# Optimization experiments

Hardware: AMD Instinct MI355X
Metric: run time of the kernel (lower is better)

The kernel has to match this reference:

```python
import jax, jax.numpy as jnp
import numpy as np

B, IMG, CIN, COUT = 8, 256, 64, 64
TILE_NUM, KSIZE = 4, 5
TILE = IMG // TILE_NUM                 # 64
FFT = KSIZE + TILE - 1                 # 68
PAD = (FFT - TILE) // 2                # 2


def setup_inputs() -> dict:
    key = jax.random.key(0)
    kx, kk = jax.random.split(key)
    x = jax.random.normal(kx, (B, IMG, IMG, CIN), dtype=jnp.float32)
    # build(): spatial random kernel -> fft2d -> trainable real/imag parts
    kernel_init = jax.random.normal(kk, (COUT, CIN, FFT, FFT), dtype=jnp.float32)
    kernel_fft = jnp.fft.fft2(kernel_init.astype(jnp.complex64))
    kernel_real = jnp.real(kernel_fft).astype(jnp.float32)
    kernel_imag = jnp.imag(kernel_fft).astype(jnp.float32)
    bias = jnp.zeros((COUT,), dtype=jnp.float32)
    return {"x": x, "kernel_real": kernel_real, "kernel_imag": kernel_imag, "bias": bias}


def _stitch(parts, pad, axis):
    """Overlap-add concat of tiles along `axis` with `pad` overlapping pixels."""
    parts = [jnp.moveaxis(p, axis, -1) for p in parts]
    out = parts[0]
    for p in parts[1:]:
        out = jnp.concatenate(
            [out[..., :-pad], out[..., -pad:] + p[..., :pad], p[..., pad:]], axis=-1)
    return jnp.moveaxis(out, -1, axis)


def reference(x, kernel_real, kernel_imag, bias):
    # x: [B, H, W, Cin] NHWC. Extract non-overlapping TILE x TILE tiles
    # (extract_glimpse centered at tile centers == plain tiling).
    b = x.shape[0]
    tiles = x.reshape(b, TILE_NUM, TILE, TILE_NUM, TILE, CIN)
    tiles = tiles.transpose(0, 1, 3, 5, 2, 4)            # [B, tr, tc, Cin, T, T]
    # pad_to_bounding_box: place tile at (PAD, PAD) inside FFT x FFT canvas
    tiles = jnp.pad(tiles, ((0, 0), (0, 0), (0, 0), (0, 0), (PAD, PAD), (PAD, PAD)))
    tiles_fft = jnp.fft.fft2(tiles.astype(jnp.complex64))  # [B, tr, tc, Cin, F, F]
    kfreq = jax.lax.complex(kernel_real, kernel_imag)      # [Cout, Cin, F, F]
    # complex multiply + reduce over input channels
    out_fft = jnp.einsum('brcihw,oihw->brcohw', tiles_fft, kfreq)
    out_tiles = jnp.real(jnp.fft.ifft2(out_fft)) + bias[:, None, None]  # [B,tr,tc,Cout,F,F]
    # overlap-add stitch: columns (last axis) then rows (axis -2)
    rows = [_stitch([out_tiles[:, r, c] for c in range(TILE_NUM)], PAD, axis=-1)
            for r in range(TILE_NUM)]
    full = _stitch(rows, PAD, axis=-2)                     # [B, Cout, Hs, Ws]
    full = full.transpose(0, 2, 3, 1)                      # NHWC
    return full[:, :IMG, :IMG, :]                          # crop_to_bounding_box(0,0,IMG,IMG)
```

## Files before the change

### kernel.cpp

```cpp
#include <hip/hip_runtime.h>
#include <hip/hip_bf16.h>


#define KH   35
#define CHS  4874240ull
#define KTB_FLOATS 9748480ull
#define WS_HEAD 34456ull

typedef float f32x4 __attribute__((ext_vector_type(4)));
typedef short s16x8 __attribute__((ext_vector_type(8)));

__device__ __forceinline__ ushort f2bf(float f) {
    __hip_bfloat16 h = __float2bfloat16(f);
    return *reinterpret_cast<ushort*>(&h);
}
__device__ __forceinline__ uint pkbf(float re, float im) {
    return (uint)f2bf(re) | ((uint)f2bf(im) << 16);
}

__global__ void k_twiddle(float* ws) {
    const float TWO_PI = 6.28318530717958647692f;
    int t = threadIdx.x;
    ushort* Wfb = (ushort*)(ws + 13976);
    for (int e = t; e < 80 * 64; e += 256) {
        int k = e >> 6, r = e & 63;
        float vr = 0.f, vi = 0.f;
        if (k < 68) {
            int ph = (k * (r + 2)) % 68;
            float a = TWO_PI * (float)ph / 68.0f;
            vr = cosf(a); vi = -sinf(a);
        }
        Wfb[e]        = f2bf(vr);
        Wfb[5120 + e] = f2bf(vi);
    }
    ushort* Wib = (ushort*)(ws + 19096);
    for (int e = t; e < 80 * 96; e += 256) {
        int p = e / 96, k = e % 96;
        float vr = 0.f, vi = 0.f;
        if (p < 68 && k < 68) {
            int ph = (p * k) % 68;
            float a = TWO_PI * (float)ph / 68.0f;
            vr = cosf(a) / 68.0f; vi = sinf(a) / 68.0f;
        }
        int dst = p * 128 + (((k >> 3) ^ (p & 7)) << 3) + (k & 7);
        Wib[dst]         = f2bf(vr);
        Wib[10240 + dst] = f2bf(vi);
    }
    ushort* Wgb = (ushort*)(ws + 29336);
    for (int e = t; e < 80 * 96; e += 256) {
        int q = e / 96, k = e % 96;
        float v = 0.f;
        if (q < 68 && k < 70) {
            int k2 = (k < KH) ? k : (k - KH);
            int ph = (q * k2) % 68;
            float a = TWO_PI * (float)ph / 68.0f;
            float alpha = (k2 == 0 || k2 == 34) ? 1.0f : 2.0f;
            v = (k < KH) ? (alpha * cosf(a) / 68.0f)
                         : (-alpha * sinf(a) / 68.0f);
        }
        int dst = q * 128 + (((k >> 3) ^ (q & 7)) << 3) + (k & 7);
        Wgb[dst] = f2bf(v);
    }
}

__global__ void k_zero_seams(float* out) {
    int b = blockIdx.x / 12, line = blockIdx.x % 12;
    const int seam[6] = {66, 67, 132, 133, 198, 199};
    int t = threadIdx.x;
    if (line < 6) {
        int y = seam[line];
        float4* dst = (float4*)(out + ((size_t)(b * 256 + y)) * 256 * 64);
        for (int e = t; e < 4096; e += 256) dst[e] = make_float4(0, 0, 0, 0);
    } else {
        int x = seam[line - 6];
        float4* dst = (float4*)out;
        for (int e = t; e < 4096; e += 256) {
            int y = e >> 4, f = e & 15;
            dst[(((size_t)(b * 256 + y)) * 256 + x) * 16 + f] = make_float4(0, 0, 0, 0);
        }
    }
}

__global__ __launch_bounds__(256) void k_kprep(
        const float* __restrict__ kr, const float* __restrict__ ki,
        ushort* __restrict__ Ktb) {
    __shared__ float sW[64 * 137];
    int k1p = blockIdx.x % 34, o = blockIdx.x / 34;
    int t = threadIdx.x;
    f32x4 vr[9], vi[9];
    #pragma unroll
    for (int j = 0; j < 9; ++j) {
        int e = t + j * 256;
        if (e < 2176) {
            int ii = e / 34, f = e % 34;
            size_t g = (size_t)(o * 64 + ii) * 4624 + (size_t)k1p * 136 + f * 4;
            vr[j] = *(const f32x4*)(kr + g);
            vi[j] = *(const f32x4*)(ki + g);
        }
    }
    #pragma unroll
    for (int j = 0; j < 9; ++j) {
        int e = t + j * 256;
        if (e < 2176) {
            int ii = e / 34, f = e % 34;
            float* d = sW + ii * 137 + f * 4;
            d[0] = vr[j][0]; d[1] = vr[j][1]; d[2] = vr[j][2]; d[3] = vr[j][3];
        }
    }
    __syncthreads();
    for (int e = t; e < 2 * KH * 64; e += 256) {
        int k1l = e / 2240, rem = e % 2240;
        int k2 = rem >> 6, i = rem & 63;
        int sw = (((i >> 3) ^ (o & 7)) << 3) | (i & 7);
        size_t dst = ((size_t)((2 * k1p + k1l) * KH + k2)) * 8192
                     + (size_t)o * 64 + sw;
        Ktb[dst] = f2bf(sW[i * 137 + k1l * 68 + k2]);
    }
    __syncthreads();
    #pragma unroll
    for (int j = 0; j < 9; ++j) {
        int e = t + j * 256;
        if (e < 2176) {
            int ii = e / 34, f = e % 34;
            float* d = sW + ii * 137 + f * 4;
            d[0] = vi[j][0]; d[1] = vi[j][1]; d[2] = vi[j][2]; d[3] = vi[j][3];
        }
    }
    __syncthreads();
    for (int e = t; e < 2 * KH * 64; e += 256) {
        int k1l = e / 2240, rem = e % 2240;
        int k2 = rem >> 6, i = rem & 63;
        int sw = (((i >> 3) ^ (o & 7)) << 3) | (i & 7);
        size_t dst = ((size_t)((2 * k1p + k1l) * KH + k2)) * 8192
                     + 4096 + (size_t)o * 64 + sw;
        Ktb[dst] = f2bf(sW[i * 137 + k1l * 68 + k2]);
    }
}

__global__ __launch_bounds__(512) void k_fwd_row(
        const float* __restrict__ x, const ushort* __restrict__ Wfb,
        uint* __restrict__ Y, int c0) {
    __shared__ __align__(16) ushort sAr[48 * 64];
    __shared__ __align__(16) ushort sAi[48 * 64];
    __shared__ __align__(16) ushort sB[4 * 64 * 64];
    int gid = blockIdx.x;
    int lc = gid >> 8;
    int rem = gid & 255;
    int nl = rem >> 4, rq = rem & 15;
    int n = (c0 + lc) * 16 + nl;
    int b = n >> 4, tr = (n >> 2) & 3, tc = n & 3;
    int t = threadIdx.x;
    for (int e = t; e < 3072; e += 512) {
        int m = e >> 6, c = e & 63;
        int sw = (m << 6) + (((c >> 3) ^ (m & 7)) << 3) + (c & 7);
        sAr[sw] = Wfb[e];
        sAi[sw] = Wfb[5120 + e];
    }
    for (int e = t; e < 4096; e += 512) {
        int rr = e >> 10, f = e & 1023;
        int c = f >> 4, i0 = (f & 15) << 2;
        int y = tr * 64 + rq * 4 + rr;
        const float4* src = (const float4*)(x + ((size_t)(b * 256 + y) * 256
                                                 + tc * 64) * 64 + (c << 6) + i0);
        float4 v = *src;
        float vv[4] = {v.x, v.y, v.z, v.w};
        #pragma unroll
        for (int u = 0; u < 4; ++u) {
            int i = i0 + u;
            sB[(rr << 12) + (i << 6) + (((c >> 3) ^ (i & 7)) << 3) + (c & 7)]
                = f2bf(vv[u]);
        }
    }
    __syncthreads();
    uint* Yc = Y + (size_t)lc * CHS;
    int lane = t & 63, w = t >> 6;
    int lm = lane & 15, kg = lane >> 4;
    int ba0 = ((kg ^ (lm & 7)) << 3);
    int ba1 = (((kg + 4) ^ (lm & 7)) << 3);
    for (int tid = w; tid < 48; tid += 8) {
        int rr = tid / 12, rem2 = tid % 12;
        int mt = rem2 >> 2, nt = rem2 & 3;
        int am = mt * 16 + lm, bn = nt * 16 + lm;
        s16x8 a0r = *(const s16x8*)(sAr + (am << 6) + ba0);
        s16x8 a1r = *(const s16x8*)(sAr + (am << 6) + ba1);
        s16x8 a0i = *(const s16x8*)(sAi + (am << 6) + ba0);
        s16x8 a1i = *(const s16x8*)(sAi + (am << 6) + ba1);
        s16x8 b0 = *(const s16x8*)(sB + (rr << 12) + (bn << 6) + ba0);
        s16x8 b1 = *(const s16x8*)(sB + (rr << 12) + (bn << 6) + ba1);
        f32x4 yr = {0.f, 0.f, 0.f, 0.f}, yi = yr;
        yr = __builtin_amdgcn_mfma_f32_16x16x32_bf16(a0r, b0, yr, 0, 0, 0);
        yr = __builtin_amdgcn_mfma_f32_16x16x32_bf16(a1r, b1, yr, 0, 0, 0);
        yi = __builtin_amdgcn_mfma_f32_16x16x32_bf16(a0i, b0, yi, 0, 0, 0);
        yi = __builtin_amdgcn_mfma_f32_16x16x32_bf16(a1i, b1, yi, 0, 0, 0);
        int r = rq * 4 + rr;
        #pragma unroll
        for (int g2 = 0; g2 < 4; ++g2) {
            int k2 = mt * 16 + kg * 4 + g2;
            if (k2 < KH)
                Yc[((size_t)(nl * KH + k2) * 64 + r) * 64 + nt * 16 + lm]
                    = pkbf(yr[g2], yi[g2]);
        }
    }
}

__global__ __launch_bounds__(512) void k_fwd_col(
        const uint* __restrict__ Y, const ushort* __restrict__ Wfb,
        uint* __restrict__ X) {
    __shared__ __align__(16) ushort sAr[80 * 64];
    __shared__ __align__(16) ushort sAi[80 * 64];
    __shared__ __align__(16) ushort sBr[64 * 64];
    __shared__ __align__(16) ushort sBi[64 * 64];
    int lc = blockIdx.x / 560;
    int rem = blockIdx.x % 560;
    int nl = rem / KH, k2 = rem % KH;
    const uint* Yg = Y + (size_t)lc * CHS + ((size_t)(nl * KH + k2)) * 4096;
    uint* Xc = X + (size_t)lc * CHS;
    int t = threadIdx.x;
    for (int e = t; e < 5120; e += 512) {
        int m = e >> 6, r = e & 63;
        int sw = (m << 6) + ((((r >> 3) ^ (m & 7))) << 3) + (r & 7);
        sAr[sw] = Wfb[e];
        sAi[sw] = Wfb[5120 + e];
    }
    for (int e = t; e < 4096; e += 512) {
        int i = e & 63, r = e >> 6;
        uint v = Yg[e];
        int sw = (i << 6) + ((((r >> 3) ^ (i & 7))) << 3) + (r & 7);
        sBr[sw] = (ushort)(v & 0xffff);
        sBi[sw] = (ushort)(v >> 16);
    }
    __syncthreads();
    int lane = t & 63, w = t >> 6;
    int lm = lane & 15, kg = lane >> 4;
    int ba0 = ((kg ^ (lm & 7)) << 3);
    int ba1 = (((kg + 4) ^ (lm & 7)) << 3);
    for (int tid = w; tid < 20; tid += 8) {
        int mt = tid >> 2, nt = tid & 3;
        int am = mt * 16 + lm, bn = nt * 16 + lm;
        s16x8 ar0 = *(const s16x8*)(sAr + (am << 6) + ba0);
        s16x8 ar1 = *(const s16x8*)(sAr + (am << 6) + ba1);
        s16x8 ai0 = *(const s16x8*)(sAi + (am << 6) + ba0);
        s16x8 ai1 = *(const s16x8*)(sAi + (am << 6) + ba1);
        s16x8 br0 = *(const s16x8*)(sBr + (bn << 6) + ba0);
        s16x8 br1 = *(const s16x8*)(sBr + (bn << 6) + ba1);
        s16x8 bi0 = *(const s16x8*)(sBi + (bn << 6) + ba0);
        s16x8 bi1 = *(const s16x8*)(sBi + (bn << 6) + ba1);
        f32x4 rr = {0.f, 0.f, 0.f, 0.f}, ii = rr, ri = rr, ir = rr;
        rr = __builtin_amdgcn_mfma_f32_16x16x32_bf16(ar0, br0, rr, 0, 0, 0);
        rr = __builtin_amdgcn_mfma_f32_16x16x32_bf16(ar1, br1, rr, 0, 0, 0);
        ii = __builtin_amdgcn_mfma_f32_16x16x32_bf16(ai0, bi0, ii, 0, 0, 0);
        ii = __builtin_amdgcn_mfma_f32_16x16x32_bf16(ai1, bi1, ii, 0, 0, 0);
        ri = __builtin_amdgcn_mfma_f32_16x16x32_bf16(ar0, bi0, ri, 0, 0, 0);
        ri = __builtin_amdgcn_mfma_f32_16x16x32_bf16(ar1, bi1, ri, 0, 0, 0);
        ir = __builtin_amdgcn_mfma_f32_16x16x32_bf16(ai0, br0, ir, 0, 0, 0);
        ir = __builtin_amdgcn_mfma_f32_16x16x32_bf16(ai1, br1, ir, 0, 0, 0);
        #pragma unroll
        for (int g2 = 0; g2 < 4; ++g2) {
            int k1 = mt * 16 + kg * 4 + g2;
            if (k1 < 68)
                Xc[((size_t)(nl * 68 + k1) * KH + k2) * 64 + nt * 16 + lm]
                    = pkbf(rr[g2] - ii[g2], ri[g2] + ir[g2]);
        }
    }
}

__global__ __launch_bounds__(256) void k_mix(
        const uint* __restrict__ X, const ushort* __restrict__ Ktb,
        uint* __restrict__ O, int CH) {
    __shared__ __align__(16) ushort sAr[16 * 64];
    __shared__ __align__(16) ushort sAi[16 * 64];
    __shared__ __align__(16) ushort sB[2 * 64 * 64];
    int bin = blockIdx.x;
    int k1 = bin / KH, k2 = bin % KH;
    int t = threadIdx.x;
    const uint4* ksrc = (const uint4*)(Ktb + (size_t)bin * 8192);
    for (int e = t; e < 1024; e += 256) ((uint4*)sB)[e] = ksrc[e];
    const ushort* sBr = sB;
    const ushort* sBi = sB + 4096;
    int lane = t & 63, w = t >> 6;
    int lm = lane & 15, kg = lane >> 4;
    for (int lc = 0; lc < CH; ++lc) {
        const uint* Xc = X + (size_t)lc * CHS;
        uint* Oc = O + (size_t)lc * CHS;
        for (int e = t; e < 1024; e += 256) {
            int n = e >> 6, i = e & 63;
            uint v = Xc[((size_t)(n * 68 + k1) * KH + k2) * 64 + i];
            int sw = (n << 6) + (((i >> 3) ^ (n & 7)) << 3) + (i & 7);
            sAr[sw] = (ushort)(v & 0xffff);
            sAi[sw] = (ushort)(v >> 16);
        }
        __syncthreads();
        f32x4 rr = {0.f, 0.f, 0.f, 0.f}, ii = rr, ri = rr, ir = rr;
        #pragma unroll
        for (int st = 0; st < 2; ++st) {
            int blk = kg + st * 4;
            int ao = (lm << 6) + ((blk ^ (lm & 7)) << 3);
            int bo = ((w * 16 + lm) << 6) + ((blk ^ (lm & 7)) << 3);
            s16x8 axr = *(const s16x8*)(sAr + ao);
            s16x8 axi = *(const s16x8*)(sAi + ao);
            s16x8 bxr = *(const s16x8*)(sBr + bo);
            s16x8 bxi = *(const s16x8*)(sBi + bo);
            rr = __builtin_amdgcn_mfma_f32_16x16x32_bf16(axr, bxr, rr, 0, 0, 0);
            ii = __builtin_amdgcn_mfma_f32_16x16x32_bf16(axi, bxi, ii, 0, 0, 0);
            ri = __builtin_amdgcn_mfma_f32_16x16x32_bf16(axr, bxi, ri, 0, 0, 0);
            ir = __builtin_amdgcn_mfma_f32_16x16x32_bf16(axi, bxr, ir, 0, 0, 0);
        }
        #pragma unroll
        for (int g2 = 0; g2 < 4; ++g2) {
            int n = kg * 4 + g2;
            int o = w * 16 + lm;
            Oc[(((size_t)n * KH + k2) * 68 + k1) * 64 + o]
                = pkbf(rr[g2] - ii[g2], ri[g2] + ir[g2]);
        }
        __syncthreads();
    }
}

__global__ __launch_bounds__(512) void k_inv_col(
        const uint* __restrict__ O, const ushort* __restrict__ Wib,
        uint* __restrict__ Z) {
    __shared__ __align__(16) ushort sAr[80 * 128];
    __shared__ __align__(16) ushort sAi[80 * 128];
    __shared__ __align__(16) ushort sBr[64 * 128];
    __shared__ __align__(16) ushort sBi[64 * 128];
    int lc = blockIdx.x / 560;
    int rem = blockIdx.x % 560;
    int nl = rem / KH, k2 = rem % KH;
    int t = threadIdx.x;
    const uint* Ob = O + (size_t)lc * CHS + ((size_t)nl * KH + k2) * 68 * 64;
    uint* Zc = Z + (size_t)lc * CHS;
    const uint4* wsrc = (const uint4*)Wib;
    for (int e = t; e < 1280; e += 512) ((uint4*)sAr)[e] = wsrc[e];
    for (int e = t; e < 1280; e += 512) ((uint4*)sAi)[e] = wsrc[1280 + e];
    uint4 zz = {0, 0, 0, 0};
    for (int e = t; e < 1024; e += 512) { ((uint4*)sBr)[e] = zz; ((uint4*)sBi)[e] = zz; }
    __syncthreads();
    for (int e = t; e < 4352; e += 512) {
        int k1 = e >> 6, o = e & 63;
        uint v = Ob[e];
        int sw = o * 128 + (((k1 >> 3) ^ (o & 7)) << 3) + (k1 & 7);
        sBr[sw] = (ushort)(v & 0xffff);
        sBi[sw] = (ushort)(v >> 16);
    }
    __syncthreads();
    int lane = t & 63, w = t >> 6;
    int lm = lane & 15, kg = lane >> 4;
    for (int tid = w; tid < 20; tid += 8) {
        int mt = tid >> 2, nt = tid & 3;
        int am = mt * 16 + lm, bn = nt * 16 + lm;
        f32x4 rr = {0.f, 0.f, 0.f, 0.f}, ii = rr, ri = rr, ir = rr;
        #pragma unroll
        for (int st = 0; st < 3; ++st) {
            int blk = kg + st * 4;
            int off = ((blk ^ (lm & 7)) << 3);
            s16x8 axr = *(const s16x8*)(sAr + am * 128 + off);
            s16x8 axi = *(const s16x8*)(sAi + am * 128 + off);
            s16x8 bxr = *(const s16x8*)(sBr + bn * 128 + off);
            s16x8 bxi = *(const s16x8*)(sBi + bn * 128 + off);
            rr = __builtin_amdgcn_mfma_f32_16x16x32_bf16(axr, bxr, rr, 0, 0, 0);
            ii = __builtin_amdgcn_mfma_f32_16x16x32_bf16(axi, bxi, ii, 0, 0, 0);
            ri = __builtin_amdgcn_mfma_f32_16x16x32_bf16(axr, bxi, ri, 0, 0, 0);
            ir = __builtin_amdgcn_mfma_f32_16x16x32_bf16(axi, bxr, ir, 0, 0, 0);
        }
        #pragma unroll
        for (int g2 = 0; g2 < 4; ++g2) {
            int p = mt * 16 + kg * 4 + g2;
            if (p < 68)
                Zc[(((size_t)(nl * 68 + p)) * KH + k2) * 64 + nt * 16 + lm]
                    = pkbf(rr[g2] - ii[g2], ri[g2] + ir[g2]);
        }
    }
}

__global__ __launch_bounds__(512) void k_fused_inv(
        const uint* __restrict__ Z, const ushort* __restrict__ Wgb,
        const float* __restrict__ bias, float* __restrict__ out, int c0) {
    __shared__ __align__(16) ushort sWg[80 * 128];
    __shared__ __align__(16) ushort sBq[2][64 * 128];
    int bid = blockIdx.x;
    int lc = bid / 272;
    int rem = bid % 272;
    int nl = rem / 17, pq = rem % 17;
    int b = c0 + lc;
    int tr = nl >> 2, tc = nl & 3;
    int t = threadIdx.x;
    const uint4* wsrc = (const uint4*)Wgb;
    for (int e = t; e < 1280; e += 512) ((uint4*)sWg)[e] = wsrc[e];
    uint4 zz = {0, 0, 0, 0};
    for (int e = t; e < 2048; e += 512) ((uint4*)sBq[0])[e] = zz;
    int lane = t & 63, w = t >> 6;
    int lm = lane & 15, kg = lane >> 4;
    float bv4[4];
    #pragma unroll
    for (int nt = 0; nt < 4; ++nt) bv4[nt] = bias[nt * 16 + lm];
    __syncthreads();
    for (int pp = 0; pp < 4; ++pp) {
        int p = pq * 4 + pp;
        int y = 66 * tr + p;
        if (y >= 256) break;
        ushort* Bq = sBq[pp & 1];
        const uint* Zb = Z + (size_t)lc * CHS + ((size_t)(nl * 68 + p)) * KH * 64;
        for (int e = t; e < KH * 64; e += 512) {
            int k2 = e >> 6, o = e & 63;
            uint v = Zb[e];
            int kb = k2 + KH;
            Bq[o * 128 + (((k2 >> 3) ^ (o & 7)) << 3) + (k2 & 7)] = (ushort)(v & 0xffff);
            Bq[o * 128 + (((kb >> 3) ^ (o & 7)) << 3) + (kb & 7)] = (ushort)(v >> 16);
        }
        __syncthreads();
        bool rowu = !((p <= 1 && tr > 0) || (p >= 66 && tr < 3));
        float* orow = out + ((size_t)(b * 256 + y)) * 256 * 64;
        for (int tid = w; tid < 20; tid += 8) {
            int mt = tid >> 2, nt = tid & 3;
            int am = mt * 16 + lm, bn = nt * 16 + lm;
            f32x4 acc = {0.f, 0.f, 0.f, 0.f};
            #pragma unroll
            for (int st = 0; st < 3; ++st) {
                int blk = kg + st * 4;
                int off = ((blk ^ (lm & 7)) << 3);
                s16x8 av = *(const s16x8*)(sWg + am * 128 + off);
                s16x8 bv = *(const s16x8*)(Bq + bn * 128 + off);
                acc = __builtin_amdgcn_mfma_f32_16x16x32_bf16(av, bv, acc, 0, 0, 0);
            }
            int o = nt * 16 + lm;
            #pragma unroll
            for (int g2 = 0; g2 < 4; ++g2) {
                int q = mt * 16 + kg * 4 + g2;
                if (q >= 68) continue;
                int xx = 66 * tc + q;
                if (xx >= 256) continue;
                bool colu = !((q <= 1 && tc > 0) || (q >= 66 && tc < 3));
                float v = acc[g2] + bv4[nt];
                float* addr = orow + (size_t)xx * 64 + o;
                if (rowu && colu) *addr = v;
                else              atomicAdd(addr, v);
            }
        }
    }
}

extern "C" void kernel_launch(void* const* d_in, const int* in_sizes, int n_in,
                              void* d_out, int out_size, void* d_ws, size_t ws_size,
                              hipStream_t stream) {
    const float* x    = (const float*)d_in[0];
    const float* kr   = (const float*)d_in[1];
    const float* ki   = (const float*)d_in[2];
    const float* bias = (const float*)d_in[3];
    float* out = (float*)d_out;
    float* ws  = (float*)d_ws;

    int CH = 4;
    while (CH > 1 && (WS_HEAD + KTB_FLOATS + 2ull * CH * CHS) * 4ull > ws_size)
        CH >>= 1;

    ushort* Wfb  = (ushort*)(ws + 13976);
    ushort* Wib  = (ushort*)(ws + 19096);
    ushort* Wgb  = (ushort*)(ws + 29336);
    ushort* Ktb  = (ushort*)(ws + WS_HEAD);
    float*  bufA = ws + WS_HEAD + KTB_FLOATS;
    float*  bufB = bufA + (size_t)CH * CHS;

    k_twiddle<<<1, 256, 0, stream>>>(ws);
    k_kprep<<<34 * 64, 256, 0, stream>>>(kr, ki, Ktb);
    k_zero_seams<<<96, 256, 0, stream>>>(out);

    for (int s = 0; s < 8; s += CH) {
        k_fwd_row<<<CH * 256, 512, 0, stream>>>(x, Wfb, (uint*)bufA, s);
        k_fwd_col<<<CH * 560, 512, 0, stream>>>((const uint*)bufA, Wfb, (uint*)bufB);
        k_mix<<<2380, 256, 0, stream>>>((const uint*)bufB, Ktb, (uint*)bufA, CH);
        k_inv_col<<<CH * 560, 512, 0, stream>>>((const uint*)bufA, Wib, (uint*)bufB);
        k_fused_inv<<<CH * 272, 512, 0, stream>>>((const uint*)bufB, Wgb, bias, out, s);
    }
}
```

Measured before the change: 366.8 us.

## Merge kernel prep into first forward-row launch and raise chunk count

Kernel-weight preparation (bf16 conversion and swizzle of the frequency-domain kernel) now runs as extra blocks of a combined launch alongside the first chunk's forward row DFT. This removes one launch and lets the two independent jobs share the GPU. The default chunk count also goes from 4 to 8 when workspace allows, so the whole batch may run in a single pass of the five-stage pipeline. That cuts launches further but needs twice the intermediate buffer memory and leaves less overlap between chunks.

```diff
diff --git a/kernel.cpp b/kernel.cpp
--- a/kernel.cpp
+++ b/kernel.cpp
@@ -81,59 +81,126 @@
     }
 }
 
-__global__ __launch_bounds__(256) void k_kprep(
+__global__ __launch_bounds__(512) void k_fused_first(
+        const float* __restrict__ x, const ushort* __restrict__ Wfb,
+        uint* __restrict__ Y,
         const float* __restrict__ kr, const float* __restrict__ ki,
-        ushort* __restrict__ Ktb) {
-    __shared__ float sW[64 * 137];
-    int k1p = blockIdx.x % 34, o = blockIdx.x / 34;
-    int t = threadIdx.x;
-    f32x4 vr[9], vi[9];
-    #pragma unroll
-    for (int j = 0; j < 9; ++j) {
-        int e = t + j * 256;
-        if (e < 2176) {
-            int ii = e / 34, f = e % 34;
-            size_t g = (size_t)(o * 64 + ii) * 4624 + (size_t)k1p * 136 + f * 4;
-            vr[j] = *(const f32x4*)(kr + g);
-            vi[j] = *(const f32x4*)(ki + g);
-        }
-    }
-    #pragma unroll
-    for (int j = 0; j < 9; ++j) {
-        int e = t + j * 256;
-        if (e < 2176) {
-            int ii = e / 34, f = e % 34;
-            float* d = sW + ii * 137 + f * 4;
-            d[0] = vr[j][0]; d[1] = vr[j][1]; d[2] = vr[j][2]; d[3] = vr[j][3];
-        }
-    }
-    __syncthreads();
-    for (int e = t; e < 2 * KH * 64; e += 256) {
-        int k1l = e / 2240, rem = e % 2240;
-        int k2 = rem >> 6, i = rem & 63;
-        int sw = (((i >> 3) ^ (o & 7)) << 3) | (i & 7);
-        size_t dst = ((size_t)((2 * k1p + k1l) * KH + k2)) * 8192
-                     + (size_t)o * 64 + sw;
-        Ktb[dst] = f2bf(sW[i * 137 + k1l * 68 + k2]);
-    }
-    __syncthreads();
-    #pragma unroll
-    for (int j = 0; j < 9; ++j) {
-        int e = t + j * 256;
-        if (e < 2176) {
-            int ii = e / 34, f = e % 34;
-            float* d = sW + ii * 137 + f * 4;
-            d[0] = vi[j][0]; d[1] = vi[j][1]; d[2] = vi[j][2]; d[3] = vi[j][3];
-        }
-    }
-    __syncthreads();
-    for (int e = t; e < 2 * KH * 64; e += 256) {
-        int k1l = e / 2240, rem = e % 2240;
-        int k2 = rem >> 6, i = rem & 63;
-        int sw = (((i >> 3) ^ (o & 7)) << 3) | (i & 7);
-        size_t dst = ((size_t)((2 * k1p + k1l) * KH + k2)) * 8192
-                     + 4096 + (size_t)o * 64 + sw;
-        Ktb[dst] = f2bf(sW[i * 137 + k1l * 68 + k2]);
+        ushort* __restrict__ Ktb, int c0, int nfr) {
+    __shared__ __align__(16) char smem[45056];
+    int t = threadIdx.x;
+    if ((int)blockIdx.x < nfr) {
+        ushort* sAr = (ushort*)smem;
+        ushort* sAi = (ushort*)(smem + 6144);
+        ushort* sB  = (ushort*)(smem + 12288);
+        int gid = blockIdx.x;
+        int lc = gid >> 8;
+        int rem = gid & 255;
+        int nl = rem >> 4, rq = rem & 15;
+        int n = (c0 + lc) * 16 + nl;
+        int b = n >> 4, tr = (n >> 2) & 3, tc = n & 3;
+        for (int e = t; e < 3072; e += 512) {
+            int m = e >> 6, c = e & 63;
+            int sw = (m << 6) + (((c >> 3) ^ (m & 7)) << 3) + (c & 7);
+            sAr[sw] = Wfb[e];
+            sAi[sw] = Wfb[5120 + e];
+        }
+        for (int e = t; e < 4096; e += 512) {
+            int rr = e >> 10, f = e & 1023;
+            int c = f >> 4, i0 = (f & 15) << 2;
+            int y = tr * 64 + rq * 4 + rr;
+            const float4* src = (const float4*)(x + ((size_t)(b * 256 + y) * 256
+                                                     + tc * 64) * 64 + (c << 6) + i0);
+            float4 v = *src;
+            float vv[4] = {v.x, v.y, v.z, v.w};
+            #pragma unroll
+            for (int u = 0; u < 4; ++u) {
+                int i = i0 + u;
+                sB[(rr << 12) + (i << 6) + (((c >> 3) ^ (i & 7)) << 3) + (c & 7)]
+                    = f2bf(vv[u]);
+            }
+        }
+        __syncthreads();
+        uint* Yc = Y + (size_t)lc * CHS;
+        int lane = t & 63, w = t >> 6;
+        int lm = lane & 15, kg = lane >> 4;
+        int ba0 = ((kg ^ (lm & 7)) << 3);
+        int ba1 = (((kg + 4) ^ (lm & 7)) << 3);
+        for (int tid = w; tid < 48; tid += 8) {
+            int rr = tid / 12, rem2 = tid % 12;
+            int mt = rem2 >> 2, nt = rem2 & 3;
+            int am = mt * 16 + lm, bn = nt * 16 + lm;
+            s16x8 a0r = *(const s16x8*)(sAr + (am << 6) + ba0);
+            s16x8 a1r = *(const s16x8*)(sAr + (am << 6) + ba1);
+            s16x8 a0i = *(const s16x8*)(sAi + (am << 6) + ba0);
+            s16x8 a1i = *(const s16x8*)(sAi + (am << 6) + ba1);
+            s16x8 b0 = *(const s16x8*)(sB + (rr << 12) + (bn << 6) + ba0);
+            s16x8 b1 = *(const s16x8*)(sB + (rr << 12) + (bn << 6) + ba1);
+            f32x4 yr = {0.f, 0.f, 0.f, 0.f}, yi = yr;
+            yr = __builtin_amdgcn_mfma_f32_16x16x32_bf16(a0r, b0, yr, 0, 0, 0);
+            yr = __builtin_amdgcn_mfma_f32_16x16x32_bf16(a1r, b1, yr, 0, 0, 0);
+            yi = __builtin_amdgcn_mfma_f32_16x16x32_bf16(a0i, b0, yi, 0, 0, 0);
+            yi = __builtin_amdgcn_mfma_f32_16x16x32_bf16(a1i, b1, yi, 0, 0, 0);
+            int r = rq * 4 + rr;
+            #pragma unroll
+            for (int g2 = 0; g2 < 4; ++g2) {
+                int k2 = mt * 16 + kg * 4 + g2;
+                if (k2 < KH)
+                    Yc[((size_t)(nl * KH + k2) * 64 + r) * 64 + nt * 16 + lm]
+                        = pkbf(yr[g2], yi[g2]);
+            }
+        }
+    } else {
+        float* sW = (float*)smem;
+        int bid = blockIdx.x - nfr;
+        int k1p = bid % 34, o = bid / 34;
+        f32x4 vr[5], vi[5];
+        #pragma unroll
+        for (int j = 0; j < 5; ++j) {
+            int e = t + j * 512;
+            if (e < 2176) {
+                int ii = e / 34, f = e % 34;
+                size_t g = (size_t)(o * 64 + ii) * 4624 + (size_t)k1p * 136 + f * 4;
+                vr[j] = *(const f32x4*)(kr + g);
+                vi[j] = *(const f32x4*)(ki + g);
+            }
+        }
+        #pragma unroll
+        for (int j = 0; j < 5; ++j) {
+            int e = t + j * 512;
+            if (e < 2176) {
+                int ii = e / 34, f = e % 34;
+                float* d = sW + ii * 137 + f * 4;
+                d[0] = vr[j][0]; d[1] = vr[j][1]; d[2] = vr[j][2]; d[3] = vr[j][3];
+            }
+        }
+        __syncthreads();
+        for (int e = t; e < 2 * KH * 64; e += 512) {
+            int k1l = e / 2240, rem = e % 2240;
+            int k2 = rem >> 6, i = rem & 63;
+            int sw = (((i >> 3) ^ (o & 7)) << 3) | (i & 7);
+            size_t dst = ((size_t)((2 * k1p + k1l) * KH + k2)) * 8192
+                         + (size_t)o * 64 + sw;
+            Ktb[dst] = f2bf(sW[i * 137 + k1l * 68 + k2]);
+        }
+        __syncthreads();
+        #pragma unroll
+        for (int j = 0; j < 5; ++j) {
+            int e = t + j * 512;
+            if (e < 2176) {
+                int ii = e / 34, f = e % 34;
+                float* d = sW + ii * 137 + f * 4;
+                d[0] = vi[j][0]; d[1] = vi[j][1]; d[2] = vi[j][2]; d[3] = vi[j][3];
+            }
+        }
+        __syncthreads();
+        for (int e = t; e < 2 * KH * 64; e += 512) {
+            int k1l = e / 2240, rem = e % 2240;
+            int k2 = rem >> 6, i = rem & 63;
+            int sw = (((i >> 3) ^ (o & 7)) << 3) | (i & 7);
+            size_t dst = ((size_t)((2 * k1p + k1l) * KH + k2)) * 8192
+                         + 4096 + (size_t)o * 64 + sw;
+            Ktb[dst] = f2bf(sW[i * 137 + k1l * 68 + k2]);
+        }
     }
 }
 
@@ -449,7 +516,7 @@
     float* out = (float*)d_out;
     float* ws  = (float*)d_ws;
 
-    int CH = 4;
+    int CH = 8;
     while (CH > 1 && (WS_HEAD + KTB_FLOATS + 2ull * CH * CHS) * 4ull > ws_size)
         CH >>= 1;
 
@@ -461,11 +528,16 @@
     float*  bufB = bufA + (size_t)CH * CHS;
 
     k_twiddle<<<1, 256, 0, stream>>>(ws);
-    k_kprep<<<34 * 64, 256, 0, stream>>>(kr, ki, Ktb);
     k_zero_seams<<<96, 256, 0, stream>>>(out);
 
     for (int s = 0; s < 8; s += CH) {
-        k_fwd_row<<<CH * 256, 512, 0, stream>>>(x, Wfb, (uint*)bufA, s);
+        if (s == 0) {
+            int nfr = CH * 256;
+            k_fused_first<<<nfr + 2176, 512, 0, stream>>>(
+                x, Wfb, (uint*)bufA, kr, ki, Ktb, 0, nfr);
+        } else {
+            k_fwd_row<<<CH * 256, 512, 0, stream>>>(x, Wfb, (uint*)bufA, s);
+        }
         k_fwd_col<<<CH * 560, 512, 0, stream>>>((const uint*)bufA, Wfb, (uint*)bufB);
         k_mix<<<2380, 256, 0, stream>>>((const uint*)bufB, Ktb, (uint*)bufA, CH);
         k_inv_col<<<CH * 560, 512, 0, stream>>>((const uint*)bufA, Wib, (uint*)bufB);
```

Result: no change. 367.6 us (+0.2%).
